# Performance work log

Measured on AMD Instinct MI355X. Metric: run time of the kernel, lower is better.

Reference implementation:

```python
import jax, jax.numpy as jnp
import numpy as np

B, S = 128, 2048
INPUT_DIM, CTX_DIM = 512, 512


def setup_inputs() -> dict:
    key = jax.random.key(0)
    ks = jax.random.split(key, 9)
    s_in = 1.0 / np.sqrt(INPUT_DIM)
    s_ctx = 1.0 / np.sqrt(CTX_DIM)
    s_out = 1.0 / np.sqrt(INPUT_DIM + CTX_DIM)
    inp = {
        "input": jax.random.normal(ks[0], (B, INPUT_DIM), jnp.float32),
        "context": jax.random.normal(ks[1], (B, S, CTX_DIM), jnp.float32),
        "context_mask": jax.random.randint(ks[2], (B, S), 0, 2) > 0,  # True = masked
        # params (torch Linear stores W as [out,in]; we store [in,out] for x @ W)
        "W_in": jax.random.uniform(ks[3], (INPUT_DIM, CTX_DIM), jnp.float32, -s_in, s_in),
        "b_in": jax.random.uniform(ks[4], (CTX_DIM,), jnp.float32, -s_in, s_in),
        "W_ctx": jax.random.uniform(ks[5], (CTX_DIM, CTX_DIM), jnp.float32, -s_ctx, s_ctx),
        "b_ctx": jax.random.uniform(ks[6], (CTX_DIM,), jnp.float32, -s_ctx, s_ctx),
        "w_score": jax.random.uniform(ks[7], (CTX_DIM,), jnp.float32, -s_ctx, s_ctx),
        "W_out": jax.random.uniform(ks[8], (INPUT_DIM + CTX_DIM, INPUT_DIM), jnp.float32, -s_out, s_out),
        "b_out": jax.random.uniform(jax.random.fold_in(key, 99), (INPUT_DIM,), jnp.float32, -s_out, s_out),
    }
    # ensure at least one unmasked position per row (avoid all -inf softmax)
    inp["context_mask"] = inp["context_mask"].at[:, 0].set(False)
    return inp


def reference(input, context, context_mask, W_in, b_in, W_ctx, b_ctx, w_score, W_out, b_out):
    # input: [B, Di], context: [B, S, Dc]
    q = input @ W_in + b_in                              # [B, Dc]
    k = jnp.einsum("bsd,de->bse", context, W_ctx) + b_ctx  # [B, S, Dc]
    # additive score: v^T tanh(q + k)
    scores = jnp.einsum("bsd,d->bs", jnp.tanh(q[:, None, :] + k), w_score)  # [B, S]
    scores = jnp.where(context_mask, -jnp.inf, scores)
    attn = jax.nn.softmax(scores, axis=-1)               # [B, S]
    ctx_vec = jnp.einsum("bs,bsd->bd", attn, context)    # [B, Dc]
    x = jnp.tanh(jnp.concatenate([ctx_vec, input], axis=1) @ W_out + b_out)  # [B, Di]
    return (x, attn)
```

## Files before the change

kernel.cpp:

```cpp
#include <hip/hip_runtime.h>
#include <hip/hip_bf16.h>
#include <math.h>

#define B_  128
#define S_  2048
#define DI  512
#define DC  512

typedef __attribute__((ext_vector_type(8))) __bf16 bf16x8;
typedef __attribute__((ext_vector_type(4))) float  f32x4;
typedef __attribute__((ext_vector_type(8))) unsigned short us8;

__device__ __forceinline__ float fast_tanh(float x) {
    float e = __expf(2.f * x);
    return 1.f - 2.f * __builtin_amdgcn_rcpf(e + 1.f);
}

__device__ __forceinline__ unsigned short f2bf(float f) {
    unsigned int u = __float_as_uint(f);
    u += 0x7FFF + ((u >> 16) & 1);
    return (unsigned short)(u >> 16);
}

__device__ __forceinline__ unsigned int pk2(float a, float b) {
    union { __hip_bfloat162 h; unsigned int u; } c;
    c.h = __float22bfloat162_rn(make_float2(a, b));
    return c.u;
}

__device__ __forceinline__ float bf2f(unsigned int lo16) {
    return __uint_as_float(lo16 << 16);
}

__global__ __launch_bounds__(256) void prep_kernel(
    const float* __restrict__ input, const float* __restrict__ W_in,
    const float* __restrict__ b_in, const float* __restrict__ b_ctx,
    const float* __restrict__ W_ctx,
    float* __restrict__ qb, unsigned short* __restrict__ WtF)
{
    __shared__ float sIn[DI];
    __shared__ float part[2][128];
    const int bx = blockIdx.x, t = threadIdx.x;
    if (bx < 512) {
        int b = bx >> 2, cg = bx & 3;
        for (int i = t; i < DI; i += 256) sIn[i] = input[b * DI + i];
        __syncthreads();
        int e = cg * 128 + (t & 127);
        int dh = t >> 7;
        float a = 0.f;
        const float* wp = W_in + (size_t)(dh * 256) * DC + e;
        #pragma unroll 4
        for (int d = 0; d < 256; ++d) a += sIn[dh * 256 + d] * wp[(size_t)d * DC];
        part[dh][t & 127] = a;
        __syncthreads();
        if (t < 128) {
            int ee = cg * 128 + t;
            qb[b * DC + ee] = b_in[ee] + b_ctx[ee] + part[0][t] + part[1][t];
        }
    } else {
        int tid = (bx - 512) * 256 + t;
        int s   = tid >> 11;
        int rem = tid & 2047;
        int g   = rem >> 6;
        int l   = rem & 63;
        int c   = g * 16 + (l & 15);
        int k0  = s * 32 + (l >> 4) * 8;
        us8 wv;
        #pragma unroll
        for (int j = 0; j < 8; ++j)
            wv[j] = f2bf(W_ctx[(size_t)(k0 + j) * DC + c]);
        *(us8*)(WtF + (size_t)tid * 8) = wv;
    }
}

__device__ __forceinline__ void bfrLoad(bf16x8 (&b)[4],
                                        const unsigned short* __restrict__ WtF,
                                        int s, int w, int lane) {
    const us8* ws = (const us8*)(WtF + (((size_t)s * 32 + w * 4) * 64 + lane) * 8);
    #pragma unroll
    for (int fn = 0; fn < 4; ++fn) b[fn] = *(const bf16x8*)(ws + fn * 64);
}

__global__ __launch_bounds__(512)
__attribute__((amdgpu_waves_per_eu(4, 4)))
void score_kernel(
    const float* __restrict__ ctx,
    const unsigned short* __restrict__ WtF,
    const float* __restrict__ qb,
    const float* __restrict__ wsc,
    const int* __restrict__ mask,
    float* __restrict__ scores_ws,
    float* __restrict__ pv_ws,
    float* __restrict__ ml_ws)
{
    __shared__ __align__(16) unsigned short ctxs[64 * 512];
    __shared__ float sred[8][64];
    __shared__ float sp[64];

    const int t = threadIdx.x;
    const int row0 = blockIdx.x * 64;
    const int bidx = row0 >> 11;
    const int lane = t & 63;
    const int w = t >> 6;
    const int lr = lane & 15, half = lane >> 4;

    bf16x8 bc[4], bn[4];
    bfrLoad(bc, WtF, 0, w, lane);

    #pragma unroll
    for (int ii = 0; ii < 4; ++ii) {
        int u0 = (2 * ii) * 512 + t;
        int u1 = (2 * ii + 1) * 512 + t;
        int r0 = u0 >> 6, k0 = u0 & 63;
        int r1 = u1 >> 6, k1 = u1 & 63;
        const float4* s0 = (const float4*)(ctx + (size_t)(row0 + r0) * DC + k0 * 8);
        const float4* s1 = (const float4*)(ctx + (size_t)(row0 + r1) * DC + k1 * 8);
        float4 a0 = s0[0], b0 = s0[1];
        float4 a1 = s1[0], b1 = s1[1];
        uint4 p0 = {pk2(a0.x, a0.y), pk2(a0.z, a0.w), pk2(b0.x, b0.y), pk2(b0.z, b0.w)};
        uint4 p1 = {pk2(a1.x, a1.y), pk2(a1.z, a1.w), pk2(b1.x, b1.y), pk2(b1.z, b1.w)};
        *(uint4*)((char*)ctxs + ((r0 * 1024 + k0 * 16) ^ ((r0 & 7) << 4))) = p0;
        *(uint4*)((char*)ctxs + ((r1 * 1024 + k1 * 16) ^ ((r1 & 7) << 4))) = p1;
    }
    __syncthreads();

    f32x4 acc[4][4] = {};
    #pragma unroll 2
    for (int s = 0; s < 16; ++s) {
        if (s < 15) bfrLoad(bn, WtF, s + 1, w, lane);
        bf16x8 af[4];
        #pragma unroll
        for (int fm = 0; fm < 4; ++fm) {
            int r = fm * 16 + lr;
            af[fm] = *(const bf16x8*)((const char*)ctxs +
                        ((r * 1024 + s * 64 + half * 16) ^ ((r & 7) << 4)));
        }
        #pragma unroll
        for (int fm = 0; fm < 4; ++fm)
            #pragma unroll
            for (int fn = 0; fn < 4; ++fn)
                acc[fm][fn] = __builtin_amdgcn_mfma_f32_16x16x32_bf16(
                    af[fm], bc[fn], acc[fm][fn], 0, 0, 0);
        if (s < 15) {
            #pragma unroll
            for (int q = 0; q < 4; ++q) bc[q] = bn[q];
        }
    }

    float wv[4], qv[4];
    #pragma unroll
    for (int fn = 0; fn < 4; ++fn) {
        int j = w * 64 + fn * 16 + lr;
        wv[fn] = wsc[j];
        qv[fn] = qb[bidx * DC + j];
    }
    #pragma unroll
    for (int fm = 0; fm < 4; ++fm) {
        #pragma unroll
        for (int reg = 0; reg < 4; ++reg) {
            float ssum = 0.f;
            #pragma unroll
            for (int fn = 0; fn < 4; ++fn)
                ssum += wv[fn] * fast_tanh(qv[fn] + acc[fm][fn][reg]);
            #pragma unroll
            for (int m = 8; m >= 1; m >>= 1)
                ssum += __shfl_xor(ssum, m, 64);
            if (lr == 0)
                sred[w][fm * 16 + half * 4 + reg] = ssum;
        }
    }
    __syncthreads();

    if (t < 64) {
        float sc = sred[0][t] + sred[1][t] + sred[2][t] + sred[3][t]
                 + sred[4][t] + sred[5][t] + sred[6][t] + sred[7][t];
        if (mask[row0 + t] != 0) sc = -1e30f;
        scores_ws[row0 + t] = sc;
        float mx = sc;
        #pragma unroll
        for (int m = 32; m >= 1; m >>= 1) mx = fmaxf(mx, __shfl_xor(mx, m, 64));
        float pe = __expf(sc - mx);
        sp[t] = pe;
        float ls = pe;
        #pragma unroll
        for (int m = 32; m >= 1; m >>= 1) ls += __shfl_xor(ls, m, 64);
        if (t == 0) {
            ml_ws[blockIdx.x * 2]     = mx;
            ml_ws[blockIdx.x * 2 + 1] = ls;
        }
    }
    __syncthreads();

    float a0 = 0.f;
    #pragma unroll 8
    for (int s2 = 0; s2 < 64; ++s2) {
        unsigned int u = *(const unsigned short*)
            ((const char*)ctxs + ((s2 * 1024 + t * 2) ^ ((s2 & 7) << 4)));
        a0 += sp[s2] * bf2f(u);
    }
    pv_ws[(size_t)blockIdx.x * 512 + t] = a0;
}

__global__ __launch_bounds__(256) void tail_kernel(
    const float* __restrict__ pv, const float* __restrict__ ml,
    const float* __restrict__ scores, const float* __restrict__ input,
    const float* __restrict__ W_out, const float* __restrict__ b_out,
    float* __restrict__ x, float* __restrict__ attn)
{
    int b = blockIdx.x, hf = blockIdx.y, t = threadIdx.x;
    __shared__ float sw[32];
    __shared__ float scm[1024];
    __shared__ float mlds[2];
    if (t < 32) {
        float m = ml[(b * 32 + t) * 2];
        float l = ml[(b * 32 + t) * 2 + 1];
        float mx = m;
        #pragma unroll
        for (int mm = 16; mm >= 1; mm >>= 1) mx = fmaxf(mx, __shfl_xor(mx, mm, 64));
        float wgt = __expf(m - mx);
        sw[t] = wgt;
        float ls = wgt * l;
        #pragma unroll
        for (int mm = 16; mm >= 1; mm >>= 1) ls += __shfl_xor(ls, mm, 64);
        if (t == 0) { mlds[0] = mx; mlds[1] = 1.f / ls; }
    }
    __syncthreads();
    const float mstar = mlds[0], invL = mlds[1];

    {
        int d0 = t * 2;
        float c0 = 0.f, c1 = 0.f;
        #pragma unroll 4
        for (int j = 0; j < 32; ++j) {
            float wgt = sw[j];
            const float2 v = *(const float2*)(pv + (size_t)(b * 32 + j) * 512 + d0);
            c0 += wgt * v.x; c1 += wgt * v.y;
        }
        scm[d0] = c0 * invL; scm[d0 + 1] = c1 * invL;
    }
    for (int i = t; i < DI; i += 256) scm[512 + i] = input[b * DI + i];
    if (hf == 0) {
        #pragma unroll
        for (int k = 0; k < 8; ++k) {
            int s = k * 256 + t;
            attn[(size_t)b * S_ + s] = __expf(scores[(size_t)b * S_ + s] - mstar) * invL;
        }
    }
    __syncthreads();

    int e = hf * 256 + t;
    float a = b_out[e];
    #pragma unroll 4
    for (int d = 0; d < 1024; ++d) a += scm[d] * W_out[(size_t)d * DI + e];
    x[b * DI + e] = fast_tanh(a);
}

extern "C" void kernel_launch(void* const* d_in, const int* in_sizes, int n_in,
                              void* d_out, int out_size, void* d_ws, size_t ws_size,
                              hipStream_t stream) {
    const float* input = (const float*)d_in[0];
    const float* ctx   = (const float*)d_in[1];
    const int*   mask  = (const int*)d_in[2];
    const float* W_in  = (const float*)d_in[3];
    const float* b_in  = (const float*)d_in[4];
    const float* W_ctx = (const float*)d_in[5];
    const float* b_ctx = (const float*)d_in[6];
    const float* wsc   = (const float*)d_in[7];
    const float* W_out = (const float*)d_in[8];
    const float* b_out = (const float*)d_in[9];

    float* x_out = (float*)d_out;
    float* attn  = (float*)d_out + B_ * DI;

    const int NTILE = (B_ * S_) / 64;

    char* ws = (char*)d_ws;
    float* qb = (float*)ws;                    ws += (size_t)B_ * DC * 4;
    unsigned short* WtF = (unsigned short*)ws; ws += (size_t)DC * DC * 2;
    float* scores_ws = (float*)ws;             ws += (size_t)B_ * S_ * 4;
    float* pv_ws = (float*)ws;                 ws += (size_t)NTILE * 512 * 4;
    float* ml_ws = (float*)ws;                 ws += (size_t)NTILE * 2 * 4;

    prep_kernel<<<640, 256, 0, stream>>>(input, W_in, b_in, b_ctx, W_ctx, qb, WtF);
    score_kernel<<<NTILE, 512, 0, stream>>>(ctx, WtF, qb, wsc, mask,
                                            scores_ws, pv_ws, ml_ws);
    tail_kernel<<<dim3(B_, 2), 256, 0, stream>>>(pv_ws, ml_ws, scores_ws, input,
                                                 W_out, b_out, x_out, attn);
}
```

Baseline: 350.1 us.

## Restructure score kernel: drop B prefetch, add MFMA priority, split PV reduction

Removes the register double-buffering of W fragments and the waves_per_eu(4,4) constraint, loading B fragments directly each step. It raises wave priority around the MFMA block with s_setprio, and simplifies the context staging loop. The final P·V accumulation is split across four row groups with 8-byte LDS reads and a shared-memory reduction, replacing the per-thread 64-iteration scalar 2-byte reads. The aim is lower register pressure and better LDS bandwidth in the PV step. The cost is an extra 8 KB of LDS, one more barrier, and exposed global load latency for the W fragments.

```diff
diff --git a/kernel.cpp b/kernel.cpp
--- a/kernel.cpp
+++ b/kernel.cpp
@@ -10,6 +10,7 @@
 typedef __attribute__((ext_vector_type(8))) __bf16 bf16x8;
 typedef __attribute__((ext_vector_type(4))) float  f32x4;
 typedef __attribute__((ext_vector_type(8))) unsigned short us8;
+typedef __attribute__((ext_vector_type(4))) unsigned short us4;
 
 __device__ __forceinline__ float fast_tanh(float x) {
     float e = __expf(2.f * x);
@@ -73,17 +74,7 @@
     }
 }
 
-__device__ __forceinline__ void bfrLoad(bf16x8 (&b)[4],
-                                        const unsigned short* __restrict__ WtF,
-                                        int s, int w, int lane) {
-    const us8* ws = (const us8*)(WtF + (((size_t)s * 32 + w * 4) * 64 + lane) * 8);
-    #pragma unroll
-    for (int fn = 0; fn < 4; ++fn) b[fn] = *(const bf16x8*)(ws + fn * 64);
-}
-
-__global__ __launch_bounds__(512)
-__attribute__((amdgpu_waves_per_eu(4, 4)))
-void score_kernel(
+__global__ __launch_bounds__(512) void score_kernel(
     const float* __restrict__ ctx,
     const unsigned short* __restrict__ WtF,
     const float* __restrict__ qb,
@@ -96,6 +87,7 @@
     __shared__ __align__(16) unsigned short ctxs[64 * 512];
     __shared__ float sred[8][64];
     __shared__ float sp[64];
+    __shared__ float pvpart[4][512];
 
     const int t = threadIdx.x;
     const int row0 = blockIdx.x * 64;
@@ -104,30 +96,28 @@
     const int w = t >> 6;
     const int lr = lane & 15, half = lane >> 4;
 
-    bf16x8 bc[4], bn[4];
-    bfrLoad(bc, WtF, 0, w, lane);
-
     #pragma unroll
-    for (int ii = 0; ii < 4; ++ii) {
-        int u0 = (2 * ii) * 512 + t;
-        int u1 = (2 * ii + 1) * 512 + t;
-        int r0 = u0 >> 6, k0 = u0 & 63;
-        int r1 = u1 >> 6, k1 = u1 & 63;
-        const float4* s0 = (const float4*)(ctx + (size_t)(row0 + r0) * DC + k0 * 8);
-        const float4* s1 = (const float4*)(ctx + (size_t)(row0 + r1) * DC + k1 * 8);
-        float4 a0 = s0[0], b0 = s0[1];
-        float4 a1 = s1[0], b1 = s1[1];
-        uint4 p0 = {pk2(a0.x, a0.y), pk2(a0.z, a0.w), pk2(b0.x, b0.y), pk2(b0.z, b0.w)};
-        uint4 p1 = {pk2(a1.x, a1.y), pk2(a1.z, a1.w), pk2(b1.x, b1.y), pk2(b1.z, b1.w)};
-        *(uint4*)((char*)ctxs + ((r0 * 1024 + k0 * 16) ^ ((r0 & 7) << 4))) = p0;
-        *(uint4*)((char*)ctxs + ((r1 * 1024 + k1 * 16) ^ ((r1 & 7) << 4))) = p1;
+    for (int i = 0; i < 8; ++i) {
+        int u = i * 512 + t;
+        int r = u >> 6, kg = u & 63;
+        const float4* src = (const float4*)(ctx + (size_t)(row0 + r) * DC + kg * 8);
+        float4 va = src[0], vb = src[1];
+        unsigned int p0 = pk2(va.x, va.y), p1 = pk2(va.z, va.w);
+        unsigned int p2 = pk2(vb.x, vb.y), p3 = pk2(vb.z, vb.w);
+        uint4 pk = {p0, p1, p2, p3};
+        *(uint4*)((char*)ctxs + ((r * 1024 + kg * 16) ^ ((r & 7) << 4))) = pk;
     }
     __syncthreads();
 
     f32x4 acc[4][4] = {};
     #pragma unroll 2
     for (int s = 0; s < 16; ++s) {
-        if (s < 15) bfrLoad(bn, WtF, s + 1, w, lane);
+        bf16x8 bfr[4];
+        const us8* wsrc = (const us8*)(WtF +
+            (((size_t)s * 32 + w * 4) * 64 + lane) * 8);
+        #pragma unroll
+        for (int fn = 0; fn < 4; ++fn)
+            bfr[fn] = *(const bf16x8*)(wsrc + fn * 64);
         bf16x8 af[4];
         #pragma unroll
         for (int fm = 0; fm < 4; ++fm) {
@@ -135,16 +125,14 @@
             af[fm] = *(const bf16x8*)((const char*)ctxs +
                         ((r * 1024 + s * 64 + half * 16) ^ ((r & 7) << 4)));
         }
+        __builtin_amdgcn_s_setprio(1);
         #pragma unroll
         for (int fm = 0; fm < 4; ++fm)
             #pragma unroll
             for (int fn = 0; fn < 4; ++fn)
                 acc[fm][fn] = __builtin_amdgcn_mfma_f32_16x16x32_bf16(
-                    af[fm], bc[fn], acc[fm][fn], 0, 0, 0);
-        if (s < 15) {
-            #pragma unroll
-            for (int q = 0; q < 4; ++q) bc[q] = bn[q];
-        }
+                    af[fm], bfr[fn], acc[fm][fn], 0, 0, 0);
+        __builtin_amdgcn_s_setprio(0);
     }
 
     float wv[4], qv[4];
@@ -191,14 +179,27 @@
     }
     __syncthreads();
 
-    float a0 = 0.f;
-    #pragma unroll 8
-    for (int s2 = 0; s2 < 64; ++s2) {
-        unsigned int u = *(const unsigned short*)
-            ((const char*)ctxs + ((s2 * 1024 + t * 2) ^ ((s2 & 7) << 4)));
-        a0 += sp[s2] * bf2f(u);
-    }
-    pv_ws[(size_t)blockIdx.x * 512 + t] = a0;
+    {
+        const int rh = t >> 7;
+        const int cg = t & 127;
+        float a0 = 0.f, a1 = 0.f, a2 = 0.f, a3 = 0.f;
+        #pragma unroll 4
+        for (int s2 = 0; s2 < 16; ++s2) {
+            int r = rh * 16 + s2;
+            float pw = sp[r];
+            us4 u = *(const us4*)((const char*)ctxs +
+                        ((r * 1024 + cg * 8) ^ ((r & 7) << 4)));
+            a0 += pw * bf2f(u[0]);
+            a1 += pw * bf2f(u[1]);
+            a2 += pw * bf2f(u[2]);
+            a3 += pw * bf2f(u[3]);
+        }
+        float4 o = {a0, a1, a2, a3};
+        *(float4*)&pvpart[rh][cg * 4] = o;
+    }
+    __syncthreads();
+    pv_ws[(size_t)blockIdx.x * 512 + t] =
+        pvpart[0][t] + pvpart[1][t] + pvpart[2][t] + pvpart[3][t];
 }
 
 __global__ __launch_bounds__(256) void tail_kernel(
```

New measurement: 346.0 us. About the same (-1.2%).
